# Performance work log

Measured on AMD Instinct MI355X. Metric: run time of the kernel, lower is better.

The kernel has to match this reference:

```python
import jax, jax.numpy as jnp
import numpy as np
from jax import lax

S, B, K, T = 16, 16, 3, 20
FP, DP = 64, 28
CP = FP - DP + 1            # 37
P = CP * CP                 # 1369 == num_pixels
H, Hh, D = 256, 128, 2


def setup_inputs() -> dict:
    key = jax.random.key(0)
    ks = jax.random.split(key, 20)

    def lin_w(k, fan_in, fan_out):
        return jax.random.normal(k, (fan_in, fan_out), jnp.float32) / np.sqrt(fan_in)

    inp = {
        "frames": jax.random.uniform(ks[0], (B, T, FP, FP), jnp.float32),
        "digit": jax.random.uniform(ks[1], (S, B, K, DP, DP), jnp.float32),
        # enc_hidden: Linear(P, H)
        "w_h1": lin_w(ks[2], P, H), "b_h1": jnp.zeros((H,), jnp.float32),
        # where_mean: Linear(H, Hh) -> ReLU -> Linear(Hh, D) -> Tanh
        "wm1": lin_w(ks[3], H, Hh), "bm1": jnp.zeros((Hh,), jnp.float32),
        "wm2": lin_w(ks[4], Hh, D), "bm2": jnp.zeros((D,), jnp.float32),
        # where_log_std: Linear(H, Hh) -> ReLU -> Linear(Hh, D)
        "ws1": lin_w(ks[5], H, Hh), "bs1": jnp.zeros((Hh,), jnp.float32),
        "ws2": lin_w(ks[6], Hh, D), "bs2": jnp.zeros((D,), jnp.float32),
        # disp_mean: Linear(P, H) -> ReLU -> Linear(H, Hh) -> ReLU -> Linear(Hh, D) -> Tanh
        "wd1": lin_w(ks[7], P, H), "bd1": jnp.zeros((H,), jnp.float32),
        "wd2": lin_w(ks[8], H, Hh), "bd2": jnp.zeros((Hh,), jnp.float32),
        "wd3": lin_w(ks[9], Hh, D), "bd3": jnp.zeros((D,), jnp.float32),
    }
    return inp


def _lin(x, w, b):
    return x @ w + b


def _forward(frames, digit, w_h1, b_h1, wm1, bm1, wm2, bm2,
             ws1, bs1, ws2, bs2, wd1, bd1, wd2, bd2, wd3, bd3):
    # frames: (B, T, FP, FP); digit: (S, B, K, DP, DP)
    s, b, k_ = digit.shape[0], digit.shape[1], digit.shape[2]
    t = frames.shape[1]

    # Template correlation. The original builds a (T, S*B*K, FP, FP) repeated
    # input and runs conv2d with groups=S*B*K. Since frames do not depend on
    # (s, k), the identical math is a grouped conv with groups=B where group b
    # holds the S*K templates for batch element b.
    x = frames.transpose(1, 0, 2, 3)                          # (T, B, FP, FP)
    kern = digit.transpose(1, 0, 2, 3, 4).reshape(b * s * k_, 1, DP, DP)
    conv = lax.conv_general_dilated(
        x, kern, window_strides=(1, 1), padding='VALID',
        dimension_numbers=('NCHW', 'OIHW', 'NCHW'),
        feature_group_count=b)                                # (T, B*S*K, CP, CP)
    cp = conv.shape[-1]
    conv = conv.reshape(t, b, s, k_, cp * cp)
    conv = conv.transpose(2, 1, 0, 3, 4)                      # (S, B, T, K, P)

    # temporal displacement of correlation maps
    conv_disp = conv[:, :, 1:] - conv[:, :, :-1]              # (S, B, T-1, K, P)

    # disp_mean MLP
    d = jax.nn.relu(_lin(conv_disp, wd1, bd1))
    d = jax.nn.relu(_lin(d, wd2, bd2))
    disp = jnp.tanh(_lin(d, wd3, bd3))                        # (S, B, T-1, K, D)

    # enc_hidden on softmax-normalized correlation maps
    hidden = jax.nn.relu(_lin(jax.nn.softmax(conv, axis=-1), w_h1, b_h1))

    q_mean = jnp.tanh(_lin(jax.nn.relu(_lin(hidden, wm1, bm1)), wm2, bm2))
    q_std = jnp.exp(_lin(jax.nn.relu(_lin(hidden, ws1, bs1)), ws2, bs2))
    return q_mean, q_std, disp


def reference(frames, digit, w_h1, b_h1, wm1, bm1, wm2, bm2,
              ws1, bs1, ws2, bs2, wd1, bd1, wd2, bd2, wd3, bd3):
    return _forward(frames, digit, w_h1, b_h1, wm1, bm1, wm2, bm2,
                    ws1, bs1, ws2, bs2, wd1, bd1, wd2, bd2, wd3, bd3)
```

## Files before the change

kernel.cpp:

```cpp
#include <hip/hip_runtime.h>
#include <hip/hip_fp16.h>

typedef __attribute__((ext_vector_type(8))) _Float16 half8;
typedef __attribute__((ext_vector_type(2))) _Float16 h2f;
typedef __attribute__((ext_vector_type(4))) float f32x4;

#define NP 1369
#define KP 1376
#define NKT 43
#define ROWS_A 15360
#define ROWS_D 14592

#define PA_OFF   0
#define PD_OFF   (ROWS_A * KP)
#define PWH_OFF  (PD_OFF + ROWS_D * KP)
#define PWD_OFF  (PWH_OFF + NKT * 16 * 512)
#define PW2_OFF  (PWD_OFF + NKT * 16 * 512)
#define PWD2_OFF (PW2_OFF + 8 * 16 * 512)
#define TSUM_OFF (PWD2_OFF + 8 * 8 * 512)

#define SHIFT_DW 2384

__device__ __forceinline__ unsigned short f2h(float f) {
    __half h = __float2half(f);
    return __half_as_ushort(h);
}
__device__ __forceinline__ h2f u2h2(unsigned int u) {
    h2f r; __builtin_memcpy(&r, &u, 4); return r;
}

__global__ __launch_bounds__(256)
void k0_pack(const float* __restrict__ w_h1, const float* __restrict__ wd1,
             const float* __restrict__ wm1,  const float* __restrict__ ws1,
             const float* __restrict__ wd2,  const float* __restrict__ digit,
             unsigned short* __restrict__ wsu, float* __restrict__ tsum)
{
    const int tid = threadIdx.x;
    if (blockIdx.x >= 3136) {
        const int sbk = (blockIdx.x - 3136) * 4 + (tid >> 6);
        const int l = tid & 63;
        const float* tp = digit + (size_t)sbk * 784;
        float s = 0.f;
        for (int i = l; i < 784; i += 64) s += tp[i];
        for (int o = 32; o; o >>= 1) s += __shfl_xor(s, o, 64);
        if (l == 0) tsum[sbk] = 0.5f * s;
        return;
    }
    int idx = blockIdx.x * 256 + tid;
    int local, mode;
    unsigned short* dst;
    if (idx < 352256)      { mode = 0; local = idx;          dst = wsu + PWH_OFF; }
    else if (idx < 704512) { mode = 1; local = idx - 352256; dst = wsu + PWD_OFF; }
    else if (idx < 770048) { mode = 2; local = idx - 704512; dst = wsu + PW2_OFF; }
    else                   { mode = 3; local = idx - 770048; dst = wsu + PWD2_OFF; }
    int j = local & 7, lane = (local >> 3) & 63, rest = local >> 9;
    int NTn = (mode == 3) ? 8 : 16;
    int nt = rest % NTn, kt = rest / NTn;
    int k = kt * 32 + ((lane >> 4) << 3) + j;
    int n = nt * 16 + (lane & 15);
    float v = 0.f;
    if (mode == 0)      { if (k < NP) v = w_h1[k * 256 + n]; }
    else if (mode == 1) { if (k < NP) v = wd1[k * 256 + n]; }
    else if (mode == 2) { v = (n < 128) ? wm1[k * 128 + n] : ws1[k * 128 + (n - 128)]; }
    else                { v = wd2[k * 128 + n]; }
    dst[local] = f2h(v);
}

__global__ __launch_bounds__(512)
void k1a_corr(const float* __restrict__ frames, const float* __restrict__ digit,
              const float* __restrict__ tsum, unsigned short* __restrict__ wsu)
{
    __shared__ __align__(16) unsigned short Bs[7 * 3 * 512];
    __shared__ __align__(16) unsigned int frd[SHIFT_DW + 64 * 37];
    __shared__ float Cn[48];

    const int tid = threadIdx.x, l = tid & 63, w = tid >> 6;
    const int mh = blockIdx.x & 1;
    const int bt = blockIdx.x >> 1;
    const int t  = bt % 20;
    const int bb = bt / 20;

    if (tid < 48) {
        int sbk_n = ((tid / 3) * 16 + bb) * 3 + (tid % 3);
        Cn[tid] = tsum[sbk_n];
    }
    if (tid < 320) {
        int r = tid / 5, d2 = tid - r * 5;
        frd[r * 37 + 32 + d2] = 0u;
        frd[SHIFT_DW + r * 37 + 32 + d2] = 0u;
    }
    {
        const float4* fp4 = (const float4*)(frames + (size_t)(bb * 20 + t) * 4096);
        for (int idx = tid; idx < 1024; idx += 512) {
            float4 v = fp4[idx];
            int r = idx >> 4, c4 = idx & 15;
            unsigned lo = (unsigned)f2h(v.x) | ((unsigned)f2h(v.y) << 16);
            unsigned hi = (unsigned)f2h(v.z) | ((unsigned)f2h(v.w) << 16);
            frd[r * 37 + c4 * 2]     = lo;
            frd[r * 37 + c4 * 2 + 1] = hi;
        }
    }
    __syncthreads();
    for (int i = tid; i < 64 * 34; i += 512) {
        int r = i / 34, d = i - r * 34;
        unsigned lo = frd[r * 37 + d], hi = frd[r * 37 + d + 1];
        frd[SHIFT_DW + r * 37 + d] = (lo >> 16) | (hi << 16);
    }

    const int c15 = l & 15, quad = l >> 4, v0q = quad << 3;
    const int cnt = (50 - w) / 8;

    int baseb[6];
#pragma unroll
    for (int it = 0; it < 6; ++it) {
        int tI = mh * 43 + w + 8 * it;
        int p  = tI * 16 + c15;
        int pc = p > 1368 ? 1368 : p;
        int i  = pc / 37;
        int jj = pc - i * 37;
        int c  = jj + v0q;
        baseb[it] = (c & 1) * (SHIFT_DW * 4) + i * 148 + ((c >> 1) << 2);
    }
    f32x4 acc[6][3];
#pragma unroll
    for (int it = 0; it < 6; ++it)
#pragma unroll
        for (int nt = 0; nt < 3; ++nt) acc[it][nt] = (f32x4){0.f, 0.f, 0.f, 0.f};

    for (int ph = 0; ph < 4; ++ph) {
        __syncthreads();
        for (int s = tid; s < 1344; s += 512) {
            int ktl = s / 192;
            int rem = s - ktl * 192;
            int nt = rem >> 6, sl = rem & 63;
            int nl = nt * 16 + (sl & 15);
            int v0 = (sl >> 4) << 3;
            int kt = ph * 7 + ktl;
            int sbk_n = ((nl / 3) * 16 + bb) * 3 + (nl % 3);
            const float* tp = digit + (size_t)sbk_n * 784 + kt * 28 + v0;
            float4 fa = *(const float4*)tp;
            float4 fb = (v0 <= 16) ? *(const float4*)(tp + 4) : make_float4(0.f, 0.f, 0.f, 0.f);
            uint4 pk;
            pk.x = (unsigned)f2h(fa.x) | ((unsigned)f2h(fa.y) << 16);
            pk.y = (unsigned)f2h(fa.z) | ((unsigned)f2h(fa.w) << 16);
            pk.z = (unsigned)f2h(fb.x) | ((unsigned)f2h(fb.y) << 16);
            pk.w = (unsigned)f2h(fb.z) | ((unsigned)f2h(fb.w) << 16);
            *(uint4*)(Bs + s * 8) = pk;
        }
        __syncthreads();

        for (int ktl = 0; ktl < 7; ++ktl) {
            const int kt = ph * 7 + ktl;
            half8 bf0 = *(const half8*)(Bs + ktl * 1536 + 0 * 512 + l * 8);
            half8 bf1 = *(const half8*)(Bs + ktl * 1536 + 1 * 512 + l * 8);
            half8 bf2 = *(const half8*)(Bs + ktl * 1536 + 2 * 512 + l * 8);
            const char* fb2 = (const char*)frd + (size_t)kt * 148;
#pragma unroll
            for (int it = 0; it < 6; ++it) {
                if (it < cnt) {
                    const unsigned* ap = (const unsigned*)(fb2 + baseb[it]);
                    union { unsigned u[4]; half8 h8; } af;
                    af.u[0] = ap[0];
                    af.u[1] = ap[1];
                    af.u[2] = ap[2];
                    af.u[3] = ap[3];
                    acc[it][0] = __builtin_amdgcn_mfma_f32_16x16x32_f16(af.h8, bf0, acc[it][0], 0, 0, 0);
                    acc[it][1] = __builtin_amdgcn_mfma_f32_16x16x32_f16(af.h8, bf1, acc[it][1], 0, 0, 0);
                    acc[it][2] = __builtin_amdgcn_mfma_f32_16x16x32_f16(af.h8, bf2, acc[it][2], 0, 0, 0);
                }
            }
        }
    }

    for (int itg = 0; itg < 6; ++itg) {
        __syncthreads();
        if (itg < cnt) {
#pragma unroll
            for (int nt = 0; nt < 3; ++nt) {
                const int nl = nt * 16 + c15;
                const float C = Cn[nl];
                ushort4 st;
                st.x = f2h(acc[itg][nt][0] - C);
                st.y = f2h(acc[itg][nt][1] - C);
                st.z = f2h(acc[itg][nt][2] - C);
                st.w = f2h(acc[itg][nt][3] - C);
                *(ushort4*)(Bs + nl * 136 + w * 16 + quad * 4) = st;
            }
        }
        __syncthreads();
        const int nseg = (itg == 5) ? 6 : 16;
        for (int i = tid; i < 48 * nseg; i += 512) {
            int rowl = i / nseg, seg = i - rowl * nseg;
            int sbk_n = ((rowl / 3) * 16 + bb) * 3 + (rowl % 3);
            uint4 v = *(const uint4*)(Bs + rowl * 136 + seg * 8);
            *(uint4*)(wsu + PA_OFF + (size_t)(sbk_n * 20 + t) * KP
                      + mh * 688 + itg * 128 + seg * 8) = v;
        }
    }
}

__global__ __launch_bounds__(512)
void k2_gemmAB(unsigned short* __restrict__ wsu, const float* __restrict__ b_h1)
{
    __shared__ __align__(16) unsigned short Bbuf[2][2 * 8192];
    __shared__ float2 smstats[64];

    const int tid = threadIdx.x, l = tid & 63, w = tid >> 6;
    const int c15 = l & 15, quad = l >> 4;
    const int M0 = blockIdx.x * 64;
    unsigned short* Abase = wsu + PA_OFF;
    const unsigned short* PWH = wsu + PWH_OFF;
    const unsigned short* PWD = wsu + PWD_OFF;
    float* HR = (float*)(wsu + PD_OFF);

    const bool isH = (w < 4);
    const int wl = w & 3;
    const int row0 = M0 + wl * 16 + c15;
    const unsigned short* a0p = Abase + (size_t)row0 * KP + quad * 8;

    for (int rr = 0; rr < 8; ++rr) {
        const int lrow = w * 8 + rr;
        const unsigned* rp = (const unsigned*)(Abase + (size_t)(M0 + lrow) * KP);
        float f0[11], f1[11];
        float mx = -3.0e38f;
#pragma unroll
        for (int i = 0; i < 11; ++i) {
            int q = l + i * 64;
            unsigned u = (q < 685) ? rp[q] : 0u;
            h2f h = u2h2(u);
            f0[i] = (q < 685) ? (float)h[0] : -3.0e38f;
            f1[i] = (q < 684) ? (float)h[1] : -3.0e38f;
            mx = fmaxf(mx, fmaxf(f0[i], f1[i]));
        }
        for (int o = 32; o; o >>= 1) mx = fmaxf(mx, __shfl_xor(mx, o, 64));
        float sum = 0.f;
#pragma unroll
        for (int i = 0; i < 11; ++i)
            sum += __expf(f0[i] - mx) + __expf(f1[i] - mx);
        for (int o = 32; o; o >>= 1) sum += __shfl_xor(sum, o, 64);
        if (l == 0) smstats[lrow] = make_float2(mx, 1.0f / sum);
    }

    f32x4 acc[16];
#pragma unroll
    for (int n = 0; n < 16; ++n) acc[n] = (f32x4){0.f, 0.f, 0.f, 0.f};

    {
        const int4* sH = (const int4*)(PWH);
        const int4* sD = (const int4*)(PWD);
        int4* dH = (int4*)(Bbuf[0]);
        int4* dD = (int4*)(Bbuf[0] + 8192);
#pragma unroll
        for (int c = 0; c < 2; ++c) {
            dH[tid + 512 * c] = sH[tid + 512 * c];
            dD[tid + 512 * c] = sD[tid + 512 * c];
        }
    }
    half8 curA = *(const half8*)(a0p);
    __syncthreads();

    float2 st0 = make_float2(0.f, 0.f);
    if (isH) st0 = smstats[wl * 16 + c15];

    for (int kt = 0; kt < NKT; ++kt) {
        const int db = kt & 1;
        half8 nxtA = curA;
        if (kt + 1 < NKT) nxtA = *(const half8*)(a0p + (kt + 1) * 32);
        int4 rH[2], rD[2];
        if (kt + 1 < NKT) {
            const int4* sH = (const int4*)(PWH + (size_t)(kt + 1) * 8192);
            const int4* sD = (const int4*)(PWD + (size_t)(kt + 1) * 8192);
#pragma unroll
            for (int c = 0; c < 2; ++c) {
                rH[c] = sH[tid + 512 * c];
                rD[c] = sD[tid + 512 * c];
            }
        }
        half8 af = curA;
        if (isH) {
            union { half8 h8; unsigned u[4]; } ia, oa;
            ia.h8 = af;
#pragma unroll
            for (int q = 0; q < 4; ++q) {
                h2f ha = u2h2(ia.u[q]);
                float a0 = __expf((float)ha[0] - st0.x) * st0.y;
                float a1 = __expf((float)ha[1] - st0.x) * st0.y;
                oa.u[q] = (unsigned)f2h(a0) | ((unsigned)f2h(a1) << 16);
            }
            af = oa.h8;
        }
        const unsigned short* bb = Bbuf[db] + (isH ? 0 : 8192);
#pragma unroll
        for (int nt = 0; nt < 16; ++nt) {
            half8 bf = *(const half8*)(bb + nt * 512 + l * 8);
            acc[nt] = __builtin_amdgcn_mfma_f32_16x16x32_f16(af, bf, acc[nt], 0, 0, 0);
        }
        if (kt + 1 < NKT) {
            int4* dH = (int4*)(Bbuf[db ^ 1]);
            int4* dD = (int4*)(Bbuf[db ^ 1] + 8192);
#pragma unroll
            for (int c = 0; c < 2; ++c) {
                dH[tid + 512 * c] = rH[c];
                dD[tid + 512 * c] = rD[c];
            }
        }
        curA = nxtA;
        __syncthreads();
    }

    if (isH) {
#pragma unroll
        for (int nt = 0; nt < 16; ++nt) {
            const int col = nt * 16 + c15;
            const float bv = b_h1[col];
#pragma unroll
            for (int r = 0; r < 4; ++r) {
                const int row = M0 + wl * 16 + quad * 4 + r;
                float v = acc[nt][r] + bv;
                Abase[(size_t)row * KP + col] = f2h(v > 0.f ? v : 0.f);
            }
        }
    } else {
#pragma unroll
        for (int nt = 0; nt < 16; ++nt) {
            const int col = nt * 16 + c15;
#pragma unroll
            for (int r = 0; r < 4; ++r) {
                const int row = M0 + wl * 16 + quad * 4 + r;
                HR[(size_t)row * 256 + col] = acc[nt][r];
            }
        }
    }
}

template <bool PATHA>
__global__ __launch_bounds__(256)
void k2_heads(unsigned short* __restrict__ wsu,
              const float* __restrict__ b1a, const float* __restrict__ b1b,
              const float* __restrict__ w2a, const float* __restrict__ b2a,
              const float* __restrict__ w2b, const float* __restrict__ b2b,
              const float* __restrict__ bd1, float* __restrict__ out)
{
    constexpr int NT2 = PATHA ? 16 : 8;
    constexpr int NI4 = NT2 / 4;
    __shared__ __align__(16) unsigned short Bsh[2][NT2 * 512];
    const int tid = threadIdx.x, l = tid & 63, w = tid >> 6;
    const int c = l & 15, quad = l >> 4;
    const int M0 = blockIdx.x * 64;
    const unsigned short* PW = wsu + (PATHA ? PW2_OFF : PWD2_OFF);

    f32x4 acc[NT2];
#pragma unroll
    for (int n = 0; n < NT2; ++n) acc[n] = (f32x4){0.f, 0.f, 0.f, 0.f};

    const int row = M0 + w * 16 + c;
    const unsigned short* arow = nullptr;
    const float* h1p = nullptr; const float* h0p = nullptr;
    if (PATHA) {
        arow = wsu + PA_OFF + (size_t)row * KP + quad * 8;
    } else {
        const float* HR = (const float*)(wsu + PD_OFF);
        const int sbk = row / 19, dt = row % 19;
        h0p = HR + (size_t)(sbk * 20 + dt) * 256 + quad * 8;
        h1p = h0p + 256;
    }

    {
        const int4* src = (const int4*)(PW);
        int4* dst = (int4*)Bsh[0];
#pragma unroll
        for (int cc = 0; cc < NI4; ++cc)
            dst[tid + 256 * cc] = src[tid + 256 * cc];
    }
    half8 curPA = {};
    float4 c1a = {}, c1b = {}, c0a = {}, c0b = {};
    if (PATHA) {
        curPA = *(const half8*)(arow);
    } else {
        c1a = *(const float4*)(h1p); c1b = *(const float4*)(h1p + 4);
        c0a = *(const float4*)(h0p); c0b = *(const float4*)(h0p + 4);
    }
    __syncthreads();

    for (int kt = 0; kt < 8; ++kt) {
        const int db = kt & 1;
        half8 nxtPA = curPA;
        float4 n1a = c1a, n1b = c1b, n0a = c0a, n0b = c0b;
        if (kt + 1 < 8) {
            if (PATHA) {
                nxtPA = *(const half8*)(arow + (kt + 1) * 32);
            } else {
                n1a = *(const float4*)(h1p + (kt + 1) * 32);
                n1b = *(const float4*)(h1p + (kt + 1) * 32 + 4);
                n0a = *(const float4*)(h0p + (kt + 1) * 32);
                n0b = *(const float4*)(h0p + (kt + 1) * 32 + 4);
            }
        }
        int4 rB[NI4];
        if (kt + 1 < 8) {
            const int4* src = (const int4*)(PW + (size_t)(kt + 1) * (NT2 * 512));
#pragma unroll
            for (int cc = 0; cc < NI4; ++cc) rB[cc] = src[tid + 256 * cc];
        }
        half8 af;
        if (PATHA) {
            af = curPA;
        } else {
            float4 bb = *(const float4*)(bd1 + kt * 32 + quad * 8);
            float4 bb2 = *(const float4*)(bd1 + kt * 32 + quad * 8 + 4);
            float v0 = fmaxf(c1a.x - c0a.x + bb.x, 0.f);
            float v1 = fmaxf(c1a.y - c0a.y + bb.y, 0.f);
            float v2 = fmaxf(c1a.z - c0a.z + bb.z, 0.f);
            float v3 = fmaxf(c1a.w - c0a.w + bb.w, 0.f);
            float v4 = fmaxf(c1b.x - c0b.x + bb2.x, 0.f);
            float v5 = fmaxf(c1b.y - c0b.y + bb2.y, 0.f);
            float v6 = fmaxf(c1b.z - c0b.z + bb2.z, 0.f);
            float v7 = fmaxf(c1b.w - c0b.w + bb2.w, 0.f);
            union { unsigned u[4]; half8 h8; } pk;
            pk.u[0] = (unsigned)f2h(v0) | ((unsigned)f2h(v1) << 16);
            pk.u[1] = (unsigned)f2h(v2) | ((unsigned)f2h(v3) << 16);
            pk.u[2] = (unsigned)f2h(v4) | ((unsigned)f2h(v5) << 16);
            pk.u[3] = (unsigned)f2h(v6) | ((unsigned)f2h(v7) << 16);
            af = pk.h8;
        }
#pragma unroll
        for (int nt = 0; nt < NT2; ++nt) {
            half8 bf = *(const half8*)(Bsh[db] + nt * 512 + l * 8);
            acc[nt] = __builtin_amdgcn_mfma_f32_16x16x32_f16(af, bf, acc[nt], 0, 0, 0);
        }
        if (kt + 1 < 8) {
            int4* dst = (int4*)Bsh[db ^ 1];
#pragma unroll
            for (int cc = 0; cc < NI4; ++cc) dst[tid + 256 * cc] = rB[cc];
        }
        curPA = nxtPA;
        c1a = n1a; c1b = n1b; c0a = n0a; c0b = n0b;
        __syncthreads();
    }
#pragma unroll
    for (int nt = 0; nt < NT2; ++nt) {
        float bv;
        if (PATHA) bv = (nt < 8) ? b1a[nt * 16 + c] : b1b[(nt - 8) * 16 + c];
        else       bv = b1a[nt * 16 + c];
#pragma unroll
        for (int r = 0; r < 4; ++r) {
            float v = acc[nt][r] + bv;
            acc[nt][r] = v > 0.f ? v : 0.f;
        }
    }
    float pm[2][4], ps[2][4];
#pragma unroll
    for (int d = 0; d < 2; ++d)
#pragma unroll
        for (int r = 0; r < 4; ++r) { pm[d][r] = 0.f; ps[d][r] = 0.f; }
#pragma unroll
    for (int d = 0; d < 2; ++d)
#pragma unroll
        for (int nt = 0; nt < 8; ++nt) {
            const float wmv = w2a[(nt * 16 + c) * 2 + d];
            float wsv = 0.f;
            if (PATHA) wsv = w2b[(nt * 16 + c) * 2 + d];
#pragma unroll
            for (int r = 0; r < 4; ++r) {
                pm[d][r] = fmaf(acc[nt][r], wmv, pm[d][r]);
                if (PATHA) ps[d][r] = fmaf(acc[nt + 8][r], wsv, ps[d][r]);
            }
        }
#pragma unroll
    for (int o = 1; o < 16; o <<= 1)
#pragma unroll
        for (int d = 0; d < 2; ++d)
#pragma unroll
            for (int r = 0; r < 4; ++r) {
                pm[d][r] += __shfl_xor(pm[d][r], o, 64);
                if (PATHA) ps[d][r] += __shfl_xor(ps[d][r], o, 64);
            }
    if (c == 0) {
#pragma unroll
        for (int r = 0; r < 4; ++r) {
            const int orow = M0 + w * 16 + quad * 4 + r;
            if (PATHA) {
                const int sbk = orow / 20, t = orow % 20;
                const int sb = sbk / 3, kk = sbk % 3;
                const int oi = ((sb * 20 + t) * 3 + kk) * 2;
                out[oi + 0] = tanhf(pm[0][r] + b2a[0]);
                out[oi + 1] = tanhf(pm[1][r] + b2a[1]);
                out[30720 + oi + 0] = __expf(ps[0][r] + b2b[0]);
                out[30720 + oi + 1] = __expf(ps[1][r] + b2b[1]);
            } else {
                const int sbk = orow / 19, dt = orow % 19;
                const int sb = sbk / 3, kk = sbk % 3;
                const int oi = 61440 + ((sb * 19 + dt) * 3 + kk) * 2;
                out[oi + 0] = tanhf(pm[0][r] + b2a[0]);
                out[oi + 1] = tanhf(pm[1][r] + b2a[1]);
            }
        }
    }
}

extern "C" void kernel_launch(void* const* d_in, const int* in_sizes, int n_in,
                              void* d_out, int out_size, void* d_ws, size_t ws_size,
                              hipStream_t stream) {
    const float* frames = (const float*)d_in[0];
    const float* digit  = (const float*)d_in[1];
    const float* w_h1   = (const float*)d_in[2];
    const float* b_h1   = (const float*)d_in[3];
    const float* wm1    = (const float*)d_in[4];
    const float* bm1    = (const float*)d_in[5];
    const float* wm2    = (const float*)d_in[6];
    const float* bm2    = (const float*)d_in[7];
    const float* ws1    = (const float*)d_in[8];
    const float* bs1    = (const float*)d_in[9];
    const float* ws2    = (const float*)d_in[10];
    const float* bs2    = (const float*)d_in[11];
    const float* wd1    = (const float*)d_in[12];
    const float* bd1    = (const float*)d_in[13];
    const float* wd2    = (const float*)d_in[14];
    const float* bd2    = (const float*)d_in[15];
    const float* wd3    = (const float*)d_in[16];
    const float* bd3    = (const float*)d_in[17];

    unsigned short* wsu = (unsigned short*)d_ws;
    float* tsum = (float*)(wsu + TSUM_OFF);
    float* o = (float*)d_out;

    k0_pack<<<dim3(3328), dim3(256), 0, stream>>>(w_h1, wd1, wm1, ws1, wd2, digit, wsu, tsum);
    k1a_corr<<<dim3(640), dim3(512), 0, stream>>>(frames, digit, tsum, wsu);
    k2_gemmAB<<<dim3(240), dim3(512), 0, stream>>>(wsu, b_h1);
    k2_heads<true><<<dim3(240), dim3(256), 0, stream>>>(wsu, bm1, bs1, wm2, bm2, ws2, bs2, nullptr, o);
    k2_heads<false><<<dim3(228), dim3(256), 0, stream>>>(wsu, bd2, nullptr, wd3, bd3, nullptr, nullptr, bd1, o);
}
```

Baseline: 128.7 us.

## Fuse where-mean/log-std heads into the hidden GEMM kernel epilogue

The hidden-layer GEMM now keeps its ReLU output tile in swizzled shared memory instead of writing it to global memory. In the same kernel it runs the second-layer MFMA GEMM against the packed where-weights, then applies the tiny output projections with tanh and exp. This removes one kernel launch plus a global write and re-read of the hidden activations. The cost is extra shared memory, which may lower occupancy, and the D-path waves sit idle during the fused stage.

Result: no change. 126.7 us (-1.6%).

```diff
diff --git a/kernel.cpp b/kernel.cpp
--- a/kernel.cpp
+++ b/kernel.cpp
@@ -200,9 +200,14 @@
 }
 
 __global__ __launch_bounds__(512)
-void k2_gemmAB(unsigned short* __restrict__ wsu, const float* __restrict__ b_h1)
+void k2_gemmAB(unsigned short* __restrict__ wsu, const float* __restrict__ b_h1,
+               const float* __restrict__ bm1, const float* __restrict__ bs1,
+               const float* __restrict__ wm2, const float* __restrict__ bm2,
+               const float* __restrict__ ws2, const float* __restrict__ bs2,
+               float* __restrict__ out)
 {
     __shared__ __align__(16) unsigned short Bbuf[2][2 * 8192];
+    __shared__ __align__(16) unsigned short Hs[64 * 264];
     __shared__ float2 smstats[64];
 
     const int tid = threadIdx.x, l = tid & 63, w = tid >> 6;
@@ -315,9 +320,10 @@
             const float bv = b_h1[col];
 #pragma unroll
             for (int r = 0; r < 4; ++r) {
-                const int row = M0 + wl * 16 + quad * 4 + r;
+                const int lrow = wl * 16 + quad * 4 + r;
+                const int csw = col ^ ((lrow & 7) << 3);
                 float v = acc[nt][r] + bv;
-                Abase[(size_t)row * KP + col] = f2h(v > 0.f ? v : 0.f);
+                Hs[lrow * 264 + csw] = f2h(v > 0.f ? v : 0.f);
             }
         }
     } else {
@@ -328,6 +334,97 @@
             for (int r = 0; r < 4; ++r) {
                 const int row = M0 + wl * 16 + quad * 4 + r;
                 HR[(size_t)row * 256 + col] = acc[nt][r];
+            }
+        }
+    }
+    __syncthreads();
+
+    const unsigned short* PW2 = wsu + PW2_OFF;
+    {
+        const int4* src = (const int4*)(PW2);
+        int4* dst = (int4*)(Bbuf[0]);
+#pragma unroll
+        for (int cc = 0; cc < 2; ++cc) dst[tid + 512 * cc] = src[tid + 512 * cc];
+    }
+    __syncthreads();
+
+    f32x4 acc2[16];
+#pragma unroll
+    for (int n = 0; n < 16; ++n) acc2[n] = (f32x4){0.f, 0.f, 0.f, 0.f};
+
+    const int hr0 = wl * 16 + c15;
+    for (int kt = 0; kt < 8; ++kt) {
+        const int db = kt & 1;
+        int4 rB2[2];
+        if (kt + 1 < 8) {
+            const int4* src = (const int4*)(PW2 + (size_t)(kt + 1) * 8192);
+#pragma unroll
+            for (int cc = 0; cc < 2; ++cc) rB2[cc] = src[tid + 512 * cc];
+        }
+        if (isH) {
+            const int hoff = (kt * 32 + quad * 8) ^ ((hr0 & 7) << 3);
+            half8 af2 = *(const half8*)(Hs + hr0 * 264 + hoff);
+#pragma unroll
+            for (int nt = 0; nt < 16; ++nt) {
+                half8 bf = *(const half8*)(Bbuf[db] + nt * 512 + l * 8);
+                acc2[nt] = __builtin_amdgcn_mfma_f32_16x16x32_f16(af2, bf, acc2[nt], 0, 0, 0);
+            }
+        }
+        if (kt + 1 < 8) {
+            int4* dst = (int4*)(Bbuf[db ^ 1]);
+#pragma unroll
+            for (int cc = 0; cc < 2; ++cc) dst[tid + 512 * cc] = rB2[cc];
+        }
+        __syncthreads();
+    }
+
+    if (isH) {
+#pragma unroll
+        for (int nt = 0; nt < 16; ++nt) {
+            float bv = (nt < 8) ? bm1[nt * 16 + c15] : bs1[(nt - 8) * 16 + c15];
+#pragma unroll
+            for (int r = 0; r < 4; ++r) {
+                float v = acc2[nt][r] + bv;
+                acc2[nt][r] = v > 0.f ? v : 0.f;
+            }
+        }
+        float pm[2][4], ps[2][4];
+#pragma unroll
+        for (int d = 0; d < 2; ++d)
+#pragma unroll
+            for (int r = 0; r < 4; ++r) { pm[d][r] = 0.f; ps[d][r] = 0.f; }
+#pragma unroll
+        for (int d = 0; d < 2; ++d)
+#pragma unroll
+            for (int nt = 0; nt < 8; ++nt) {
+                const float wmv = wm2[(nt * 16 + c15) * 2 + d];
+                const float wsv = ws2[(nt * 16 + c15) * 2 + d];
+#pragma unroll
+                for (int r = 0; r < 4; ++r) {
+                    pm[d][r] = fmaf(acc2[nt][r], wmv, pm[d][r]);
+                    ps[d][r] = fmaf(acc2[nt + 8][r], wsv, ps[d][r]);
+                }
+            }
+#pragma unroll
+        for (int o = 1; o < 16; o <<= 1)
+#pragma unroll
+            for (int d = 0; d < 2; ++d)
+#pragma unroll
+                for (int r = 0; r < 4; ++r) {
+                    pm[d][r] += __shfl_xor(pm[d][r], o, 64);
+                    ps[d][r] += __shfl_xor(ps[d][r], o, 64);
+                }
+        if (c15 == 0) {
+#pragma unroll
+            for (int r = 0; r < 4; ++r) {
+                const int orow = M0 + wl * 16 + quad * 4 + r;
+                const int sbk = orow / 20, t = orow % 20;
+                const int sb = sbk / 3, kk = sbk % 3;
+                const int oi = ((sb * 20 + t) * 3 + kk) * 2;
+                out[oi + 0] = tanhf(pm[0][r] + bm2[0]);
+                out[oi + 1] = tanhf(pm[1][r] + bm2[1]);
+                out[30720 + oi + 0] = __expf(ps[0][r] + bs2[0]);
+                out[30720 + oi + 1] = __expf(ps[1][r] + bs2[1]);
             }
         }
     }
@@ -526,7 +623,6 @@
 
     k0_pack<<<dim3(3328), dim3(256), 0, stream>>>(w_h1, wd1, wm1, ws1, wd2, digit, wsu, tsum);
     k1a_corr<<<dim3(640), dim3(512), 0, stream>>>(frames, digit, tsum, wsu);
-    k2_gemmAB<<<dim3(240), dim3(512), 0, stream>>>(wsu, b_h1);
-    k2_heads<true><<<dim3(240), dim3(256), 0, stream>>>(wsu, bm1, bs1, wm2, bm2, ws2, bs2, nullptr, o);
+    k2_gemmAB<<<dim3(240), dim3(512), 0, stream>>>(wsu, b_h1, bm1, bs1, wm2, bm2, ws2, bs2, o);
     k2_heads<false><<<dim3(228), dim3(256), 0, stream>>>(wsu, bd2, nullptr, wd3, bd3, nullptr, nullptr, bd1, o);
 }
```
